# Kernel optimization log

Hardware: AMD Instinct MI355X
Metric: run time of the kernel (lower is better)

Reference implementation:

```python
import jax, jax.numpy as jnp
import numpy as np

LEVEL = 10
S = 2 ** (LEVEL + 1)   # face side (ring size)
HS = S // 2            # half side (rows per face)
B = 2
F = 5                  # five faces of the icosahedral rhombus layout


def setup_inputs() -> dict:
    key = jax.random.key(0)
    ks = jax.random.split(key, 10)
    mk = lambda k, shp: jax.random.normal(k, shp, dtype=jnp.float32)
    return {
        "x": mk(ks[0], (B, F, HS, S)),
        "poles": mk(ks[1], (B, 2, 1)),
        "w_inner": mk(ks[2], (6, HS - 2, S - 2)),
        "w_east": mk(ks[3], (6, HS - 1)),
        "w_cn": mk(ks[4], (6,)),
        "w_ne": mk(ks[5], (6, HS - 2)),
        "w_nne": mk(ks[6], (6,)),
        "w_nw": mk(ks[7], (6, HS - 2)),
        "w_nww": mk(ks[8], (6,)),
        "w_west": mk(ks[9], (6, HS - 1)),
    }


def _wp(face_slice, xi, w):
    # wrap-previous face diff: out[f] = (in[f-1 mod 5] - x[f]) * w
    return (jnp.roll(face_slice, 1, axis=1) - xi) * w


def _wn(face_slice, xi, w):
    # wrap-next face diff: out[f] = (in[f+1 mod 5] - x[f]) * w
    return (jnp.roll(face_slice, -1, axis=1) - xi) * w


def reference(x, poles, w_inner, w_east, w_cn, w_ne, w_nne, w_nw, w_nww, w_west):
    Bb, Ff, hs, s = x.shape
    out = jnp.zeros((Bb, 4, Ff, hs, s), x.dtype)

    # ---- interior patch (all neighbors in-face) ----
    xi = x[:, :, 1:-1, 1:-1]                                  # [B,5,HS-2,S-2]
    d0 = (x[:, :, :-2, :-2] - xi) * w_inner[0]
    d1 = (x[:, :, 2:, 2:] - xi) * w_inner[1]
    d2 = (x[:, :, :-2, 1:-1] - xi) * w_inner[2] + (x[:, :, 1:-1, 2:] - xi) * w_inner[3]
    d3 = (x[:, :, 1:-1, :-2] - xi) * w_inner[4] + (x[:, :, 2:, 1:-1] - xi) * w_inner[5]
    out = out.at[:, :, :, 1:-1, 1:-1].set(jnp.stack([d0, d1, d2, d3], axis=1))

    # ---- east seam: row 0, cols 1:HS ----
    xi = x[:, :, 0, 1:hs]                                     # [B,5,HS-1]
    d0 = _wp(x[:, :, hs - 1, hs:s - 1], xi, w_east[0])
    d1 = (x[:, :, 1, 2:hs + 1] - xi) * w_east[1]
    d2 = _wp(x[:, :, hs - 1, hs + 1:s], xi, w_east[2]) + (x[:, :, 0, 2:hs + 1] - xi) * w_east[3]
    d3 = (x[:, :, 0, 0:hs - 1] - xi) * w_east[4] + (x[:, :, 1, 1:hs] - xi) * w_east[5]
    out = out.at[:, :, :, 0, 1:hs].set(jnp.stack([d0, d1, d2, d3], axis=1))

    # ---- corner-north vertex: row 0, col HS ----
    xi = x[:, :, 0, hs]                                       # [B,5]
    d0 = _wp(x[:, :, hs - 1, s - 1], xi, w_cn[0])
    d1 = (x[:, :, 1, hs + 1] - xi) * w_cn[1]
    d2 = (x[:, :, 0, hs + 1] - xi) * w_cn[2]
    d3 = (x[:, :, 0, hs - 1] - xi) * w_cn[3] + (x[:, :, 1, hs] - xi) * w_cn[4]
    out = out.at[:, :, :, 0, hs].set(jnp.stack([d0, d1, d2, d3], axis=1))

    # ---- north-east seam: row 0, cols HS+1:S-1 ----
    xi = x[:, :, 0, hs + 1:s - 1]                             # [B,5,HS-2]
    d0 = _wp(x[:, :, hs - 2:0:-1, s - 1], xi, w_ne[0]) + _wp(x[:, :, hs - 1:1:-1, s - 1], xi, w_ne[1])
    d1 = (x[:, :, 1, hs + 2:s] - xi) * w_ne[2] + (x[:, :, 1, hs + 1:s - 1] - xi) * w_ne[3]
    d2 = (x[:, :, 0, hs + 2:s] - xi) * w_ne[4]
    d3 = (x[:, :, 0, hs:s - 2] - xi) * w_ne[5]
    out = out.at[:, :, :, 0, hs + 1:s - 1].set(jnp.stack([d0, d1, d2, d3], axis=1))

    # ---- north-north-east corner (touches pole): row 0, col S-1 ----
    xi = x[:, :, 0, s - 1]                                    # [B,5]
    d0 = _wp(x[:, :, 0, s - 1], xi, w_nne[0]) + _wp(x[:, :, 1, s - 1], xi, w_nne[1])
    d1 = _wn(x[:, :, 0, s - 1], xi, w_nne[2]) + (x[:, :, 1, s - 1] - xi) * w_nne[3]
    d2 = (poles[:, 1] - xi) * w_nne[4]
    d3 = (x[:, :, 0, s - 2] - xi) * w_nne[5]
    out = out.at[:, :, :, 0, s - 1].set(jnp.stack([d0, d1, d2, d3], axis=1))

    # ---- north-west seam: rows 1:HS-1, col S-1 ----
    xi = x[:, :, 1:hs - 1, s - 1]                             # [B,5,HS-2]
    d0 = (x[:, :, 0:hs - 2, s - 2] - xi) * w_nw[0]
    d1 = _wn(x[:, :, 0, s - 2:hs:-1], xi, w_nw[1])
    d2 = (x[:, :, 0:hs - 2, s - 1] - xi) * w_nw[2] + _wn(x[:, :, 0, s - 1:hs + 1:-1], xi, w_nw[3])
    d3 = (x[:, :, 1:hs - 1, s - 2] - xi) * w_nw[4] + (x[:, :, 2:hs, s - 1] - xi) * w_nw[5]
    out = out.at[:, :, :, 1:hs - 1, s - 1].set(jnp.stack([d0, d1, d2, d3], axis=1))

    # ---- north-west-west corner: row HS-1, col S-1 ----
    xi = x[:, :, hs - 1, s - 1]                               # [B,5]
    d0 = (x[:, :, hs - 2, s - 2] - xi) * w_nww[0]
    d1 = _wn(x[:, :, 0, hs], xi, w_nww[1])
    d2 = (x[:, :, hs - 2, s - 1] - xi) * w_nww[2] + _wn(x[:, :, 0, hs + 1], xi, w_nww[3])
    d3 = (x[:, :, hs - 1, s - 2] - xi) * w_nww[4] + _wn(x[:, :, 0, hs - 1], xi, w_nww[5])
    out = out.at[:, :, :, hs - 1, s - 1].set(jnp.stack([d0, d1, d2, d3], axis=1))

    # ---- west seam: row HS-1, cols HS:S-1 ----
    xi = x[:, :, hs - 1, hs:s - 1]                            # [B,5,HS-1]
    d0 = (x[:, :, hs - 2, hs - 1:s - 2] - xi) * w_west[0]
    d1 = _wn(x[:, :, 0, 1:hs], xi, w_west[1])
    d2 = (x[:, :, hs - 2, hs:s - 1] - xi) * w_west[2] + (x[:, :, hs - 1, hs + 1:s] - xi) * w_west[3]
    d3 = (x[:, :, hs - 1, hs - 1:s - 2] - xi) * w_west[4] + _wn(x[:, :, 0, 0:hs - 1], xi, w_west[5])
    out = out.at[:, :, :, hs - 1, hs:s - 1].set(jnp.stack([d0, d1, d2, d3], axis=1))

    return out
```

## Files before the change

### kernel.cpp

```cpp
#include <hip/hip_runtime.h>

constexpr int S  = 2048;
constexpr int HS = 1024;
constexpr int B  = 2;
constexpr int F  = 5;
constexpr int PL = HS * S;
constexpr int OD = F * PL;
constexpr int WI = (HS - 2) * (S - 2);

constexpr int NPLANE = B * F;
constexpr int INTERIOR_BLOCKS = 8 * 128 * NPLANE * 2;

typedef float v4  __attribute__((ext_vector_type(4)));
typedef float v4u __attribute__((ext_vector_type(4), aligned(4)));

__device__ __forceinline__ void st_nt(float* p, v4 v) {
    __builtin_nontemporal_store(v, (v4*)p);
}
__device__ __forceinline__ v4 ldu(const float* p) {
    return *(const v4u*)p;
}

__device__ void scalar_point(
    int i, int j,
    const float* __restrict__ x, const float* __restrict__ poles,
    const float* __restrict__ w_inner, const float* __restrict__ w_east,
    const float* __restrict__ w_cn, const float* __restrict__ w_ne,
    const float* __restrict__ w_nne, const float* __restrict__ w_nw,
    const float* __restrict__ w_nww, const float* __restrict__ w_west,
    float* __restrict__ out)
{
    if (j == 0 || (i == HS - 1 && j < HS)) {
        for (int b = 0; b < B; ++b) {
#pragma unroll
            for (int f = 0; f < F; ++f) {
                float* ob = out + b * (4 * OD) + f * PL + i * S + j;
                ob[0] = 0.f; ob[OD] = 0.f; ob[2 * OD] = 0.f; ob[3 * OD] = 0.f;
            }
        }
        return;
    }

    if (i > 0 && i < HS - 1 && j < S - 1) {
        const int wo = (i - 1) * (S - 2) + (j - 1);
        const float w0 = w_inner[wo];
        const float w1 = w_inner[wo + WI];
        const float w2 = w_inner[wo + 2 * WI];
        const float w3 = w_inner[wo + 3 * WI];
        const float w4 = w_inner[wo + 4 * WI];
        const float w5 = w_inner[wo + 5 * WI];
        const int rm = (i - 1) * S + j;
        const int rc = i * S + j;
        const int rp = (i + 1) * S + j;
        for (int b = 0; b < B; ++b) {
#pragma unroll
            for (int f = 0; f < F; ++f) {
                const float* xb = x + (b * F + f) * PL;
                const float xi = xb[rc];
                const float d0 = (xb[rm - 1] - xi) * w0;
                const float d1 = (xb[rp + 1] - xi) * w1;
                const float d2 = (xb[rm] - xi) * w2 + (xb[rc + 1] - xi) * w3;
                const float d3 = (xb[rc - 1] - xi) * w4 + (xb[rp] - xi) * w5;
                float* ob = out + b * (4 * OD) + f * PL + rc;
                ob[0] = d0; ob[OD] = d1; ob[2 * OD] = d2; ob[3 * OD] = d3;
            }
        }
        return;
    }

    if (i == 0) {
        if (j < HS) {
            const int t = j - 1;
            const float w0 = w_east[t];
            const float w1 = w_east[t + (HS - 1)];
            const float w2 = w_east[t + 2 * (HS - 1)];
            const float w3 = w_east[t + 3 * (HS - 1)];
            const float w4 = w_east[t + 4 * (HS - 1)];
            const float w5 = w_east[t + 5 * (HS - 1)];
            for (int b = 0; b < B; ++b) {
#pragma unroll
                for (int f = 0; f < F; ++f) {
                    const int fm = (f == 0) ? F - 1 : f - 1;
                    const float* xb  = x + (b * F + f) * PL;
                    const float* xmb = x + (b * F + fm) * PL;
                    const float xi = xb[j];
                    const float d0 = (xmb[(HS - 1) * S + HS + t] - xi) * w0;
                    const float d1 = (xb[S + 2 + t] - xi) * w1;
                    const float d2 = (xmb[(HS - 1) * S + HS + 1 + t] - xi) * w2
                                   + (xb[2 + t] - xi) * w3;
                    const float d3 = (xb[t] - xi) * w4 + (xb[S + 1 + t] - xi) * w5;
                    float* ob = out + b * (4 * OD) + f * PL + j;
                    ob[0] = d0; ob[OD] = d1; ob[2 * OD] = d2; ob[3 * OD] = d3;
                }
            }
        } else if (j == HS) {
            const float w0 = w_cn[0], w1 = w_cn[1], w2 = w_cn[2], w3 = w_cn[3], w4 = w_cn[4];
            for (int b = 0; b < B; ++b) {
#pragma unroll
                for (int f = 0; f < F; ++f) {
                    const int fm = (f == 0) ? F - 1 : f - 1;
                    const float* xb  = x + (b * F + f) * PL;
                    const float* xmb = x + (b * F + fm) * PL;
                    const float xi = xb[HS];
                    const float d0 = (xmb[(HS - 1) * S + S - 1] - xi) * w0;
                    const float d1 = (xb[S + HS + 1] - xi) * w1;
                    const float d2 = (xb[HS + 1] - xi) * w2;
                    const float d3 = (xb[HS - 1] - xi) * w3 + (xb[S + HS] - xi) * w4;
                    float* ob = out + b * (4 * OD) + f * PL + HS;
                    ob[0] = d0; ob[OD] = d1; ob[2 * OD] = d2; ob[3 * OD] = d3;
                }
            }
        } else if (j < S - 1) {
            const int t = j - HS - 1;
            const float w0 = w_ne[t];
            const float w1 = w_ne[t + (HS - 2)];
            const float w2 = w_ne[t + 2 * (HS - 2)];
            const float w3 = w_ne[t + 3 * (HS - 2)];
            const float w4 = w_ne[t + 4 * (HS - 2)];
            const float w5 = w_ne[t + 5 * (HS - 2)];
            for (int b = 0; b < B; ++b) {
#pragma unroll
                for (int f = 0; f < F; ++f) {
                    const int fm = (f == 0) ? F - 1 : f - 1;
                    const float* xb  = x + (b * F + f) * PL;
                    const float* xmb = x + (b * F + fm) * PL;
                    const float xi = xb[j];
                    const float d0 = (xmb[(HS - 2 - t) * S + S - 1] - xi) * w0
                                   + (xmb[(HS - 1 - t) * S + S - 1] - xi) * w1;
                    const float d1 = (xb[S + HS + 2 + t] - xi) * w2
                                   + (xb[S + HS + 1 + t] - xi) * w3;
                    const float d2 = (xb[HS + 2 + t] - xi) * w4;
                    const float d3 = (xb[HS + t] - xi) * w5;
                    float* ob = out + b * (4 * OD) + f * PL + j;
                    ob[0] = d0; ob[OD] = d1; ob[2 * OD] = d2; ob[3 * OD] = d3;
                }
            }
        } else {
            const float w0 = w_nne[0], w1 = w_nne[1], w2 = w_nne[2],
                        w3 = w_nne[3], w4 = w_nne[4], w5 = w_nne[5];
            for (int b = 0; b < B; ++b) {
#pragma unroll
                for (int f = 0; f < F; ++f) {
                    const int fm = (f == 0) ? F - 1 : f - 1;
                    const int fp = (f == F - 1) ? 0 : f + 1;
                    const float* xb  = x + (b * F + f) * PL;
                    const float* xmb = x + (b * F + fm) * PL;
                    const float* xpb = x + (b * F + fp) * PL;
                    const float xi = xb[S - 1];
                    const float d0 = (xmb[S - 1] - xi) * w0 + (xmb[S + S - 1] - xi) * w1;
                    const float d1 = (xpb[S - 1] - xi) * w2 + (xb[S + S - 1] - xi) * w3;
                    const float d2 = (poles[b * 2 + 1] - xi) * w4;
                    const float d3 = (xb[S - 2] - xi) * w5;
                    float* ob = out + b * (4 * OD) + f * PL + (S - 1);
                    ob[0] = d0; ob[OD] = d1; ob[2 * OD] = d2; ob[3 * OD] = d3;
                }
            }
        }
        return;
    }

    if (i == HS - 1) {
        if (j < S - 1) {
            const int t = j - HS;
            const float w0 = w_west[t];
            const float w1 = w_west[t + (HS - 1)];
            const float w2 = w_west[t + 2 * (HS - 1)];
            const float w3 = w_west[t + 3 * (HS - 1)];
            const float w4 = w_west[t + 4 * (HS - 1)];
            const float w5 = w_west[t + 5 * (HS - 1)];
            for (int b = 0; b < B; ++b) {
#pragma unroll
                for (int f = 0; f < F; ++f) {
                    const int fp = (f == F - 1) ? 0 : f + 1;
                    const float* xb  = x + (b * F + f) * PL;
                    const float* xpb = x + (b * F + fp) * PL;
                    const float xi = xb[(HS - 1) * S + j];
                    const float d0 = (xb[(HS - 2) * S + HS - 1 + t] - xi) * w0;
                    const float d1 = (xpb[1 + t] - xi) * w1;
                    const float d2 = (xb[(HS - 2) * S + HS + t] - xi) * w2
                                   + (xb[(HS - 1) * S + HS + 1 + t] - xi) * w3;
                    const float d3 = (xb[(HS - 1) * S + HS - 1 + t] - xi) * w4
                                   + (xpb[t] - xi) * w5;
                    float* ob = out + b * (4 * OD) + f * PL + (HS - 1) * S + j;
                    ob[0] = d0; ob[OD] = d1; ob[2 * OD] = d2; ob[3 * OD] = d3;
                }
            }
        } else {
            const float w0 = w_nww[0], w1 = w_nww[1], w2 = w_nww[2],
                        w3 = w_nww[3], w4 = w_nww[4], w5 = w_nww[5];
            for (int b = 0; b < B; ++b) {
#pragma unroll
                for (int f = 0; f < F; ++f) {
                    const int fp = (f == F - 1) ? 0 : f + 1;
                    const float* xb  = x + (b * F + f) * PL;
                    const float* xpb = x + (b * F + fp) * PL;
                    const float xi = xb[(HS - 1) * S + S - 1];
                    const float d0 = (xb[(HS - 2) * S + S - 2] - xi) * w0;
                    const float d1 = (xpb[HS] - xi) * w1;
                    const float d2 = (xb[(HS - 2) * S + S - 1] - xi) * w2
                                   + (xpb[HS + 1] - xi) * w3;
                    const float d3 = (xb[(HS - 1) * S + S - 2] - xi) * w4
                                   + (xpb[HS - 1] - xi) * w5;
                    float* ob = out + b * (4 * OD) + f * PL + (HS - 1) * S + (S - 1);
                    ob[0] = d0; ob[OD] = d1; ob[2 * OD] = d2; ob[3 * OD] = d3;
                }
            }
        }
        return;
    }

    {
        const int t = i - 1;
        const float w0 = w_nw[t];
        const float w1 = w_nw[t + (HS - 2)];
        const float w2 = w_nw[t + 2 * (HS - 2)];
        const float w3 = w_nw[t + 3 * (HS - 2)];
        const float w4 = w_nw[t + 4 * (HS - 2)];
        const float w5 = w_nw[t + 5 * (HS - 2)];
        for (int b = 0; b < B; ++b) {
#pragma unroll
            for (int f = 0; f < F; ++f) {
                const int fp = (f == F - 1) ? 0 : f + 1;
                const float* xb  = x + (b * F + f) * PL;
                const float* xpb = x + (b * F + fp) * PL;
                const float xi = xb[i * S + S - 1];
                const float d0 = (xb[(i - 1) * S + S - 2] - xi) * w0;
                const float d1 = (xpb[S - 2 - t] - xi) * w1;
                const float d2 = (xb[(i - 1) * S + S - 1] - xi) * w2
                               + (xpb[S - 1 - t] - xi) * w3;
                const float d3 = (xb[i * S + S - 2] - xi) * w4
                               + (xb[(i + 1) * S + S - 1] - xi) * w5;
                float* ob = out + b * (4 * OD) + f * PL + i * S + (S - 1);
                ob[0] = d0; ob[OD] = d1; ob[2 * OD] = d2; ob[3 * OD] = d3;
            }
        }
    }
}

__global__ __launch_bounds__(256)
void icok(const float* __restrict__ x, const float* __restrict__ poles,
          const float* __restrict__ w_inner, const float* __restrict__ w_east,
          const float* __restrict__ w_cn, const float* __restrict__ w_ne,
          const float* __restrict__ w_nne, const float* __restrict__ w_nw,
          const float* __restrict__ w_nww, const float* __restrict__ w_west,
          float* __restrict__ out)
{
    const int p = blockIdx.x;

    if (p < INTERIOR_BLOCKS) {
        const int band = p & 7;
        const int idx  = p >> 3;
        const int rowb = idx / 20;
        const int t    = idx - rowb * 20;
        const int plane = t >> 1;
        const int half  = t & 1;
        const int i = band * 128 + rowb + 1;
        if (i > HS - 2) return;
        const int jt = (half << 8) | threadIdx.x;
        if (jt == 0 || jt == 511) return;
        const int j0 = jt << 2;

        const int wo = (i - 1) * (S - 2) + (j0 - 1);
        const v4 w0v = ldu(w_inner + wo);
        const v4 w1v = ldu(w_inner + wo + WI);
        const v4 w2v = ldu(w_inner + wo + 2 * WI);
        const v4 w3v = ldu(w_inner + wo + 3 * WI);
        const v4 w4v = ldu(w_inner + wo + 4 * WI);
        const v4 w5v = ldu(w_inner + wo + 5 * WI);

        const int rm = (i - 1) * S + j0;
        const int rc = i * S + j0;
        const int rp = (i + 1) * S + j0;

        const float* xb = x + plane * PL;
        const v4 c   = *(const v4*)(xb + rc);
        const v4 m   = *(const v4*)(xb + rm);
        const v4 pv  = *(const v4*)(xb + rp);
        const v4 mm1 = ldu(xb + rm - 1);
        const v4 cm1 = ldu(xb + rc - 1);
        const v4 cp1 = ldu(xb + rc + 1);
        const v4 pp1 = ldu(xb + rp + 1);

        const v4 d0 = (mm1 - c) * w0v;
        const v4 d1 = (pp1 - c) * w1v;
        const v4 d2 = (m - c) * w2v + (cp1 - c) * w3v;
        const v4 d3 = (cm1 - c) * w4v + (pv - c) * w5v;

        const int bb = (plane >= F) ? 1 : 0;
        const int ff = plane - bb * F;
        float* ob = out + bb * (4 * OD) + ff * PL + rc;
        st_nt(ob, d0);
        st_nt(ob + OD, d1);
        st_nt(ob + 2 * OD, d2);
        st_nt(ob + 3 * OD, d3);
        return;
    }

    const int e = (p - INTERIOR_BLOCKS) * 256 + threadIdx.x;
    int i, j;
    if (e < 2048)      { i = 0;      j = e; }
    else if (e < 4096) { i = HS - 1; j = e - 2048; }
    else if (e < 4096 + 8 * (HS - 2)) {
        const int t = e - 4096;
        i = 1 + (t >> 3);
        const int c = t & 7;
        j = (c < 4) ? c : (2040 + c);
    } else return;
    scalar_point(i, j, x, poles, w_inner, w_east, w_cn, w_ne, w_nne,
                 w_nw, w_nww, w_west, out);
}

extern "C" void kernel_launch(void* const* d_in, const int* in_sizes, int n_in,
                              void* d_out, int out_size, void* d_ws, size_t ws_size,
                              hipStream_t stream) {
    const float* x       = (const float*)d_in[0];
    const float* poles   = (const float*)d_in[1];
    const float* w_inner = (const float*)d_in[2];
    const float* w_east  = (const float*)d_in[3];
    const float* w_cn    = (const float*)d_in[4];
    const float* w_ne    = (const float*)d_in[5];
    const float* w_nne   = (const float*)d_in[6];
    const float* w_nw    = (const float*)d_in[7];
    const float* w_nww   = (const float*)d_in[8];
    const float* w_west  = (const float*)d_in[9];
    float* out = (float*)d_out;

    dim3 grid(INTERIOR_BLOCKS + 48), block(256);
    hipLaunchKernelGGL(icok, grid, block, 0, stream,
                       x, poles, w_inner, w_east, w_cn, w_ne, w_nne, w_nw,
                       w_nww, w_west, out);
}
```

Measured before the change: 485.0 us.

## Loop over all planes per thread to reuse interior weights in registers

Each interior thread now loads its six weight vectors once, with nontemporal loads, and loops over all ten batch-face planes. Before, every plane's block reloaded the same weights. Edge blocks move to the front of the grid, and the grid shrinks to 2048 interior blocks with a band-interleaved row mapping. This cuts redundant weight traffic and the cache pressure it causes, but leaves fewer blocks, each doing ten times the work, with a serial unroll-1 loop that may expose memory latency.

New measurement: 464.1 us. -4.3%, faster.

```diff
diff --git a/kernel.cpp b/kernel.cpp
--- a/kernel.cpp
+++ b/kernel.cpp
@@ -9,7 +9,7 @@
 constexpr int WI = (HS - 2) * (S - 2);
 
 constexpr int NPLANE = B * F;
-constexpr int INTERIOR_BLOCKS = 8 * 128 * NPLANE * 2;
+constexpr int EDGE_BLOCKS = 48;
 
 typedef float v4  __attribute__((ext_vector_type(4)));
 typedef float v4u __attribute__((ext_vector_type(4), aligned(4)));
@@ -19,6 +19,9 @@
 }
 __device__ __forceinline__ v4 ldu(const float* p) {
     return *(const v4u*)p;
+}
+__device__ __forceinline__ v4 ldu_nt(const float* p) {
+    return __builtin_nontemporal_load((const v4u*)p);
 }
 
 __device__ void scalar_point(
@@ -247,56 +250,57 @@
 {
     const int p = blockIdx.x;
 
-    if (p < INTERIOR_BLOCKS) {
-        const int band = p & 7;
-        const int idx  = p >> 3;
-        const int rowb = idx / 20;
-        const int t    = idx - rowb * 20;
-        const int plane = t >> 1;
-        const int half  = t & 1;
-        const int i = band * 128 + rowb + 1;
+    if (p >= EDGE_BLOCKS) {
+        const int q = p - EDGE_BLOCKS;
+        const int l = ((q & 7) << 8) | (q >> 3);
+        const int i = 1 + (l >> 1);
         if (i > HS - 2) return;
-        const int jt = (half << 8) | threadIdx.x;
+        const int jt = ((l & 1) << 8) | threadIdx.x;
         if (jt == 0 || jt == 511) return;
         const int j0 = jt << 2;
 
         const int wo = (i - 1) * (S - 2) + (j0 - 1);
-        const v4 w0v = ldu(w_inner + wo);
-        const v4 w1v = ldu(w_inner + wo + WI);
-        const v4 w2v = ldu(w_inner + wo + 2 * WI);
-        const v4 w3v = ldu(w_inner + wo + 3 * WI);
-        const v4 w4v = ldu(w_inner + wo + 4 * WI);
-        const v4 w5v = ldu(w_inner + wo + 5 * WI);
+        const v4 w0v = ldu_nt(w_inner + wo);
+        const v4 w1v = ldu_nt(w_inner + wo + WI);
+        const v4 w2v = ldu_nt(w_inner + wo + 2 * WI);
+        const v4 w3v = ldu_nt(w_inner + wo + 3 * WI);
+        const v4 w4v = ldu_nt(w_inner + wo + 4 * WI);
+        const v4 w5v = ldu_nt(w_inner + wo + 5 * WI);
 
         const int rm = (i - 1) * S + j0;
         const int rc = i * S + j0;
         const int rp = (i + 1) * S + j0;
 
-        const float* xb = x + plane * PL;
-        const v4 c   = *(const v4*)(xb + rc);
-        const v4 m   = *(const v4*)(xb + rm);
-        const v4 pv  = *(const v4*)(xb + rp);
-        const v4 mm1 = ldu(xb + rm - 1);
-        const v4 cm1 = ldu(xb + rc - 1);
-        const v4 cp1 = ldu(xb + rc + 1);
-        const v4 pp1 = ldu(xb + rp + 1);
-
-        const v4 d0 = (mm1 - c) * w0v;
-        const v4 d1 = (pp1 - c) * w1v;
-        const v4 d2 = (m - c) * w2v + (cp1 - c) * w3v;
-        const v4 d3 = (cm1 - c) * w4v + (pv - c) * w5v;
-
-        const int bb = (plane >= F) ? 1 : 0;
-        const int ff = plane - bb * F;
-        float* ob = out + bb * (4 * OD) + ff * PL + rc;
-        st_nt(ob, d0);
-        st_nt(ob + OD, d1);
-        st_nt(ob + 2 * OD, d2);
-        st_nt(ob + 3 * OD, d3);
-        return;
-    }
-
-    const int e = (p - INTERIOR_BLOCKS) * 256 + threadIdx.x;
+        const float* xb = x + rc;
+        float* ob = out + rc;
+
+#pragma unroll 1
+        for (int plane = 0; plane < NPLANE; ++plane) {
+            const v4 c   = *(const v4*)(xb);
+            const v4 m   = *(const v4*)(xb + (rm - rc));
+            const v4 pv  = *(const v4*)(xb + (rp - rc));
+            const v4 mm1 = ldu(xb + (rm - rc) - 1);
+            const v4 cm1 = ldu(xb - 1);
+            const v4 cp1 = ldu(xb + 1);
+            const v4 pp1 = ldu(xb + (rp - rc) + 1);
+
+            const v4 d0 = (mm1 - c) * w0v;
+            const v4 d1 = (pp1 - c) * w1v;
+            const v4 d2 = (m - c) * w2v + (cp1 - c) * w3v;
+            const v4 d3 = (cm1 - c) * w4v + (pv - c) * w5v;
+
+            st_nt(ob, d0);
+            st_nt(ob + OD, d1);
+            st_nt(ob + 2 * OD, d2);
+            st_nt(ob + 3 * OD, d3);
+
+            xb += PL;
+            ob += (plane == F - 1) ? (4 * OD - (F - 1) * PL) : PL;
+        }
+        return;
+    }
+
+    const int e = p * 256 + threadIdx.x;
     int i, j;
     if (e < 2048)      { i = 0;      j = e; }
     else if (e < 4096) { i = HS - 1; j = e - 2048; }
@@ -325,7 +329,7 @@
     const float* w_west  = (const float*)d_in[9];
     float* out = (float*)d_out;
 
-    dim3 grid(INTERIOR_BLOCKS + 48), block(256);
+    dim3 grid(EDGE_BLOCKS + 2048), block(256);
     hipLaunchKernelGGL(icok, grid, block, 0, stream,
                        x, poles, w_inner, w_east, w_cn, w_ne, w_nne, w_nw,
                        w_nww, w_west, out);
```
